# Kernel tuning notes

Measured on AMD Instinct MI355X. Metric: run time of the kernel, lower is better.

## Reference

```python
import jax, jax.numpy as jnp
import numpy as np

T, B, N = 512, 64, 1024
H = N // 2  # per-direction RNN hidden size


def _rnn_dir(x, Wih, Whh, bih, bhh):
    """Single-direction vanilla tanh RNN. x: [T,B,N] -> hs: [T,B,H]."""
    xw = jnp.einsum('tbn,hn->tbh', x, Wih) + bih  # precompute input proj
    h0 = jnp.zeros((x.shape[1], Whh.shape[0]), x.dtype)

    def step(hprev, xt):
        h = jnp.tanh(xt + hprev @ Whh.T + bhh)
        return h, h

    _, hs = jax.lax.scan(step, h0, xw)
    return hs


def setup_inputs() -> dict:
    key = jax.random.key(0)
    ks = jax.random.split(key, 8)
    sc_in = 1.0 / np.sqrt(N)
    sc_h = 1.0 / np.sqrt(H)
    return {
        's': jax.random.normal(ks[0], (B, N), jnp.float32),
        'x': jax.random.normal(ks[1], (T, B, N), jnp.float32),
        'Wih_f': jax.random.normal(ks[2], (H, N), jnp.float32) * sc_in,
        'Whh_f': jax.random.normal(ks[3], (H, H), jnp.float32) * sc_h,
        'bih_f': jnp.zeros((H,), jnp.float32),
        'bhh_f': jnp.zeros((H,), jnp.float32),
        'Wih_b': jax.random.normal(ks[4], (H, N), jnp.float32) * sc_in,
        'Whh_b': jax.random.normal(ks[5], (H, H), jnp.float32) * sc_h,
        'bih_b': jnp.zeros((H,), jnp.float32),
        'bhh_b': jnp.zeros((H,), jnp.float32),
        'W1': jax.random.normal(ks[6], (N, 2 * N), jnp.float32) * (1.0 / np.sqrt(2 * N)),
        'b1': jnp.zeros((N,), jnp.float32),
        'W2': jax.random.normal(ks[7], (1, N), jnp.float32) * sc_in,
        'b2': jnp.zeros((1,), jnp.float32),
    }


def reference(s, x, Wih_f, Whh_f, bih_f, bhh_f, Wih_b, Whh_b, bih_b, bhh_b, W1, b1, W2, b2):
    # Bidirectional RNN: forward scan + reversed scan, concat on feature axis.
    hf = _rnn_dir(x, Wih_f, Whh_f, bih_f, bhh_f)          # [T,B,H]
    hb = _rnn_dir(x[::-1], Wih_b, Whh_b, bih_b, bhh_b)[::-1]
    h = jnp.concatenate([hf, hb], axis=-1)                # [T,B,N]

    # Batched attention scoring MLP (replaces the per-timestep Python loop):
    # e_t = tanh(W2 @ tanh(W1 @ [s; h_t] + b1) + b2)
    sb = jnp.broadcast_to(s[None], h.shape)               # [T,B,N]
    z = jnp.concatenate([sb, h], axis=-1)                 # [T,B,2N]
    e = jnp.tanh(jnp.tanh(z @ W1.T + b1) @ W2.T + b2)     # [T,B,1]

    # softmax over time (original: softmax(dim=1) on [B,T]), then weighted sum.
    a = jax.nn.softmax(e[..., 0], axis=0)                 # [T,B]
    return jnp.einsum('tb,tbn->bn', a, h)                 # [B,N]
```

## Files before the change

kernel.cpp:

```cpp
#include <hip/hip_runtime.h>

#define Tn 512
#define Bn 64
#define Nn 1024
#define Hn 512

typedef __attribute__((ext_vector_type(8))) short short8;
typedef __attribute__((ext_vector_type(4))) float f32x4;
typedef __attribute__((ext_vector_type(4))) int int4v;

__device__ __forceinline__ unsigned short f2bf_hi(float x) {
  unsigned u = __builtin_bit_cast(unsigned, x);
  unsigned r = u + 0x7FFFu + ((u >> 16) & 1u);
  return (unsigned short)(r >> 16);
}
__device__ __forceinline__ float bf2f(unsigned short b) {
  unsigned u = ((unsigned)b) << 16;
  return __builtin_bit_cast(float, u);
}


__global__ __launch_bounds__(256) void k0_sproj(const float* __restrict__ s,
    const float* __restrict__ W1, const float* __restrict__ b1,
    float* __restrict__ SP) {
  const int b = blockIdx.x;
  const int tid = threadIdx.x;
  __shared__ float sl[Nn];
  for (int i = tid; i < Nn; i += 256) sl[i] = s[(size_t)b * Nn + i];
  __syncthreads();
#pragma unroll
  for (int qq = 0; qq < 4; ++qq) {
    const int j = qq * 256 + tid;
    const float* w = W1 + (size_t)j * (2 * Nn);
    float acc = 0.f;
    for (int i = 0; i < Nn; i += 4) {
      const float4 wv = *(const float4*)(w + i);
      acc += sl[i] * wv.x + sl[i + 1] * wv.y + sl[i + 2] * wv.z + sl[i + 3] * wv.w;
    }
    SP[(size_t)b * Nn + j] = acc + b1[j];
  }
}

#define LDA 40
__global__ __launch_bounds__(256) void k1_mfma(const float* __restrict__ X,
    const float* __restrict__ Wf, const float* __restrict__ Wb,
    const float* __restrict__ bif, const float* __restrict__ bib,
    float* __restrict__ XW) {
  __shared__ __align__(16) unsigned short Ahi[128 * LDA];
  __shared__ __align__(16) unsigned short Alo[128 * LDA];
  __shared__ __align__(16) unsigned short Bhi[128 * LDA];
  __shared__ __align__(16) unsigned short Blo[128 * LDA];
  const int tid = threadIdx.x;
  const int n0 = blockIdx.x * 128;
  const int m0 = blockIdx.y * 128;
  const int lane = tid & 63;
  const int w = tid >> 6;
  const int mw = (w >> 1) * 64, nw = (w & 1) * 64;
  const int l15 = lane & 15, l4 = lane >> 4;

  const float* bsrc;
  const float* bias_base;
  if (n0 < 512) { bsrc = Wf + (size_t)n0 * Nn; bias_base = bif + n0; }
  else          { bsrc = Wb + (size_t)(n0 - 512) * Nn; bias_base = bib + (n0 - 512); }

  const int srow = tid >> 1, scol = (tid & 1) * 16;
  const float* ag = X + (size_t)(m0 + srow) * Nn + scol;
  const float* bg = bsrc + (size_t)srow * Nn + scol;

  f32x4 acc[4][4];
#pragma unroll
  for (int i = 0; i < 4; ++i)
#pragma unroll
    for (int j = 0; j < 4; ++j) acc[i][j] = (f32x4){0.f, 0.f, 0.f, 0.f};

  for (int kt = 0; kt < 32; ++kt) {
    const int k0 = kt * 32;
    float4 av[4], bv[4];
#pragma unroll
    for (int c = 0; c < 4; ++c) {
      av[c] = *(const float4*)(ag + k0 + c * 4);
      bv[c] = *(const float4*)(bg + k0 + c * 4);
    }
    __syncthreads();
#pragma unroll
    for (int c = 0; c < 4; ++c) {
      const float a4[4] = {av[c].x, av[c].y, av[c].z, av[c].w};
      const float b4[4] = {bv[c].x, bv[c].y, bv[c].z, bv[c].w};
      ushort4 ah, al, bh, bl;
      unsigned short* ahp = (unsigned short*)&ah;
      unsigned short* alp = (unsigned short*)&al;
      unsigned short* bhp = (unsigned short*)&bh;
      unsigned short* blp = (unsigned short*)&bl;
#pragma unroll
      for (int e = 0; e < 4; ++e) {
        const unsigned short h = f2bf_hi(a4[e]);
        ahp[e] = h; alp[e] = f2bf_hi(a4[e] - bf2f(h));
        const unsigned short g = f2bf_hi(b4[e]);
        bhp[e] = g; blp[e] = f2bf_hi(b4[e] - bf2f(g));
      }
      const int off = srow * LDA + scol + c * 4;
      *(ushort4*)&Ahi[off] = ah; *(ushort4*)&Alo[off] = al;
      *(ushort4*)&Bhi[off] = bh; *(ushort4*)&Blo[off] = bl;
    }
    __syncthreads();
    short8 afh[4], afl[4];
#pragma unroll
    for (int mi = 0; mi < 4; ++mi) {
      const int off = (mw + mi * 16 + l15) * LDA + l4 * 8;
      afh[mi] = *(const short8*)&Ahi[off];
      afl[mi] = *(const short8*)&Alo[off];
    }
#pragma unroll
    for (int ni = 0; ni < 4; ++ni) {
      const int off = (nw + ni * 16 + l15) * LDA + l4 * 8;
      const short8 bfh = *(const short8*)&Bhi[off];
      const short8 bfl = *(const short8*)&Blo[off];
#pragma unroll
      for (int mi = 0; mi < 4; ++mi) {
        acc[mi][ni] = __builtin_amdgcn_mfma_f32_16x16x32_bf16(afh[mi], bfh, acc[mi][ni], 0, 0, 0);
        acc[mi][ni] = __builtin_amdgcn_mfma_f32_16x16x32_bf16(afh[mi], bfl, acc[mi][ni], 0, 0, 0);
        acc[mi][ni] = __builtin_amdgcn_mfma_f32_16x16x32_bf16(afl[mi], bfh, acc[mi][ni], 0, 0, 0);
      }
    }
  }
#pragma unroll
  for (int ni = 0; ni < 4; ++ni) {
    const int col = n0 + nw + ni * 16 + l15;
    const float bias = bias_base[nw + ni * 16 + l15];
#pragma unroll
    for (int mi = 0; mi < 4; ++mi) {
      const int row = m0 + mw + mi * 16 + l4 * 4;
#pragma unroll
      for (int reg = 0; reg < 4; ++reg)
        XW[(size_t)(row + reg) * Nn + col] = acc[mi][ni][reg] + bias;
    }
  }
}

#define K2F 16
#define WAITV8 do { asm volatile("s_waitcnt vmcnt(8)" ::: "memory"); __builtin_amdgcn_sched_barrier(0); } while (0)
#define WAITV0 do { asm volatile("s_waitcnt vmcnt(0)" ::: "memory"); __builtin_amdgcn_sched_barrier(0); } while (0)
#define K2_LD(dh, dl, kt) do { \
    const unsigned short* _ph = pbh + (size_t)(kt) * 2048; \
    const unsigned short* _pl = pbl + (size_t)(kt) * 2048; \
    asm volatile("global_load_dwordx4 %0, %1, off sc0 sc1" : "=v"(dh) : "v"(_ph)); \
    asm volatile("global_load_dwordx4 %0, %1, off sc0 sc1" : "=v"(dl) : "v"(_pl)); \
  } while (0)
#define K2_MM(xh, xl, kt) do { \
    const short8 _a = __builtin_bit_cast(short8, xh); \
    const short8 _c = __builtin_bit_cast(short8, xl); \
    a0 = __builtin_amdgcn_mfma_f32_16x16x32_bf16(_a, Bh[kt], a0, 0, 0, 0); \
    a1 = __builtin_amdgcn_mfma_f32_16x16x32_bf16(_a, Bl[kt], a1, 0, 0, 0); \
    a2 = __builtin_amdgcn_mfma_f32_16x16x32_bf16(_c, Bh[kt], a2, 0, 0, 0); \
  } while (0)

__global__ __launch_bounds__(512, 1) void k2_scan_mfma(
    const float* __restrict__ XW,
    const float* __restrict__ Whh_f, const float* __restrict__ Whh_b,
    const float* __restrict__ bhh_f, const float* __restrict__ bhh_b,
    unsigned short* __restrict__ HFhi, unsigned short* __restrict__ HFlo,
    int* __restrict__ FL) {
  const int wg = blockIdx.x;
  const int dir = wg >> 4;
  const int rg = wg & 15;
  const int tid = threadIdx.x;
  const int lane = tid & 63;
  const int w = tid >> 6;
  const int m = w & 3;
  const int cg = w >> 2;
  const int l15 = lane & 15, l4 = lane >> 4;
  __shared__ __align__(16) unsigned short PKhi[2048];
  __shared__ __align__(16) unsigned short PKlo[2048];

  const float* Whh = dir ? Whh_b : Whh_f;
  const float* bhh = dir ? bhh_b : bhh_f;
  const int ocol = rg * 32 + cg * 16 + l15;

  short8 Bh[16], Bl[16];
  {
    const float* wr = Whh + (size_t)ocol * Hn;
#pragma unroll
    for (int kt = 0; kt < 16; ++kt) {
      const float4 w0 = *(const float4*)(wr + kt * 32 + l4 * 8);
      const float4 w1 = *(const float4*)(wr + kt * 32 + l4 * 8 + 4);
      const float wf[8] = {w0.x, w0.y, w0.z, w0.w, w1.x, w1.y, w1.z, w1.w};
      union { unsigned short u[8]; short8 v; } hh, ll;
#pragma unroll
      for (int e = 0; e < 8; ++e) {
        const unsigned short h = f2bf_hi(wf[e]);
        hh.u[e] = h; ll.u[e] = f2bf_hi(wf[e] - bf2f(h));
      }
      Bh[kt] = hh.v; Bl[kt] = ll.v;
    }
  }
  const float bhh_c = bhh[ocol];
  const int g2p = cg * 2 + (l15 >> 3);
  const int ep = l15 & 7;

  for (int t = 0; t < Tn; ++t) {
    const int trow = dir ? (Tn - 1 - t) : t;
    float xw0, xw1, xw2, xw3;
    {
      const float* xp = XW + ((size_t)trow * Bn + m * 16 + l4 * 4) * Nn + dir * 512 + ocol;
      const float* x0 = xp;             const float* x1 = xp + Nn;
      const float* x2 = xp + 2 * Nn;    const float* x3 = xp + 3 * Nn;
      asm volatile("global_load_dword %0, %1, off" : "=v"(xw0) : "v"(x0));
      asm volatile("global_load_dword %0, %1, off" : "=v"(xw1) : "v"(x1));
      asm volatile("global_load_dword %0, %1, off" : "=v"(xw2) : "v"(x2));
      asm volatile("global_load_dword %0, %1, off" : "=v"(xw3) : "v"(x3));
    }

    f32x4 a0 = {0.f, 0.f, 0.f, 0.f}, a1 = a0, a2 = a0;
    if (t > 0) {
      {
        int* fp = FL + (size_t)(((dir << 9) | (t - 1))) * K2F;
        while (true) {
          const int v = __hip_atomic_load(fp + (lane & 15), __ATOMIC_RELAXED,
                                          __HIP_MEMORY_SCOPE_AGENT);
          if (__all(v != 0)) break;
          __builtin_amdgcn_s_sleep(1);
        }
      }
      asm volatile("" ::: "memory");
      const int hprow = dir ? (Tn - t) : (t - 1);
      const unsigned short* pbh =
          HFhi + (size_t)(hprow * 2 + dir) * 32768 + m * 512 + lane * 8;
      const unsigned short* pbl =
          HFlo + (size_t)(hprow * 2 + dir) * 32768 + m * 512 + lane * 8;
      int4v Ph[4], Pl[4], Qh[4], Ql[4];
      K2_LD(Ph[0], Pl[0], 0);  K2_LD(Ph[1], Pl[1], 1);
      K2_LD(Ph[2], Pl[2], 2);  K2_LD(Ph[3], Pl[3], 3);
      K2_LD(Qh[0], Ql[0], 4);  K2_LD(Qh[1], Ql[1], 5);
      K2_LD(Qh[2], Ql[2], 6);  K2_LD(Qh[3], Ql[3], 7);
      WAITV8;
      K2_MM(Ph[0], Pl[0], 0);  K2_MM(Ph[1], Pl[1], 1);
      K2_MM(Ph[2], Pl[2], 2);  K2_MM(Ph[3], Pl[3], 3);
      K2_LD(Ph[0], Pl[0], 8);  K2_LD(Ph[1], Pl[1], 9);
      K2_LD(Ph[2], Pl[2], 10); K2_LD(Ph[3], Pl[3], 11);
      WAITV8;
      K2_MM(Qh[0], Ql[0], 4);  K2_MM(Qh[1], Ql[1], 5);
      K2_MM(Qh[2], Ql[2], 6);  K2_MM(Qh[3], Ql[3], 7);
      K2_LD(Qh[0], Ql[0], 12); K2_LD(Qh[1], Ql[1], 13);
      K2_LD(Qh[2], Ql[2], 14); K2_LD(Qh[3], Ql[3], 15);
      WAITV8;
      K2_MM(Ph[0], Pl[0], 8);  K2_MM(Ph[1], Pl[1], 9);
      K2_MM(Ph[2], Pl[2], 10); K2_MM(Ph[3], Pl[3], 11);
      WAITV0;
      K2_MM(Qh[0], Ql[0], 12); K2_MM(Qh[1], Ql[1], 13);
      K2_MM(Qh[2], Ql[2], 14); K2_MM(Qh[3], Ql[3], 15);
    }
    WAITV0;

#pragma unroll
    for (int reg = 0; reg < 4; ++reg) {
      const float xwv = (reg == 0) ? xw0 : (reg == 1) ? xw1 : (reg == 2) ? xw2 : xw3;
      const float pre = a0[reg] + a1[reg] + a2[reg] + xwv + bhh_c;
      const float h = tanhf(pre);
      const unsigned short hi = f2bf_hi(h);
      const unsigned short lo = f2bf_hi(h - bf2f(hi));
      const int idx = m * 512 + g2p * 128 + (l4 * 4 + reg) * 8 + ep;
      PKhi[idx] = hi;
      PKlo[idx] = lo;
    }
    __syncthreads();
    {
      const int half = tid >> 8;
      const int i = tid & 255;
      unsigned short* dst = (half ? HFlo : HFhi) +
          (size_t)(trow * 2 + dir) * 32768 + (size_t)rg * 2048 + (size_t)i * 8;
      const unsigned short* src = (half ? PKlo : PKhi) + i * 8;
      const int4v v = *(const int4v*)src;
      asm volatile("global_store_dwordx4 %0, %1, off sc0 sc1" :: "v"(dst), "v"(v) : "memory");
    }
    asm volatile("s_waitcnt vmcnt(0)" ::: "memory");
    __syncthreads();
    if (tid == 0)
      __hip_atomic_store(FL + (size_t)(((dir << 9) | t)) * K2F + rg, 1,
                         __ATOMIC_RELAXED, __HIP_MEMORY_SCOPE_AGENT);
  }
}

__global__ __launch_bounds__(256) void k3_mfma(
    const unsigned short* __restrict__ Hhi, const unsigned short* __restrict__ Hlo,
    const float* __restrict__ W1, const float* __restrict__ SP,
    const float* __restrict__ W2, float* __restrict__ EP) {
  __shared__ __align__(16) unsigned short Ahi[128 * LDA];
  __shared__ __align__(16) unsigned short Alo[128 * LDA];
  __shared__ __align__(16) unsigned short Bhi[128 * LDA];
  __shared__ __align__(16) unsigned short Blo[128 * LDA];
  __shared__ __align__(16) float SPs[64 * 128];
  const int tid = threadIdx.x;
  const int n0 = blockIdx.x * 128;
  const int m0 = blockIdx.y * 128;
  const int lane = tid & 63;
  const int w = tid >> 6;
  const int mw = (w >> 1) * 64, nw = (w & 1) * 64;
  const int l15 = lane & 15, l4 = lane >> 4;

  {
    const int r64 = tid >> 2, c0 = (tid & 3) * 32;
    const float* sps = SP + (size_t)r64 * Nn + n0 + c0;
    float* spd = &SPs[r64 * 128 + c0];
#pragma unroll
    for (int c = 0; c < 8; ++c) *(float4*)(spd + c * 4) = *(const float4*)(sps + c * 4);
  }

  const int srow = tid >> 1, scol = (tid & 1) * 16;
  const int tb = m0 + srow;
  const int t3 = tb >> 6, b3 = tb & 63;
  const size_t abase = (size_t)t3 * 65536 + (size_t)(b3 >> 4) * 512 + (size_t)(b3 & 15) * 8
                     + (size_t)(scol >> 3) * 128;
  const float* bg = W1 + (size_t)(n0 + srow) * (2 * Nn) + Nn + scol;

  f32x4 acc[4][4];
#pragma unroll
  for (int i = 0; i < 4; ++i)
#pragma unroll
    for (int j = 0; j < 4; ++j) acc[i][j] = (f32x4){0.f, 0.f, 0.f, 0.f};

  for (int kt = 0; kt < 32; ++kt) {
    const int k0 = kt * 32;
    const size_t gidx = abase + (size_t)(kt >> 4) * 32768 + (size_t)(kt & 15) * 2048;
    const short8 avh0 = *(const short8*)(Hhi + gidx);
    const short8 avh1 = *(const short8*)(Hhi + gidx + 128);
    const short8 avl0 = *(const short8*)(Hlo + gidx);
    const short8 avl1 = *(const short8*)(Hlo + gidx + 128);
    float4 bv0 = *(const float4*)(bg + k0);
    float4 bv1 = *(const float4*)(bg + k0 + 4);
    float4 bv2 = *(const float4*)(bg + k0 + 8);
    float4 bv3 = *(const float4*)(bg + k0 + 12);
    __syncthreads();
    {
      const int off = srow * LDA + scol;
      *(short8*)&Ahi[off] = avh0; *(short8*)&Ahi[off + 8] = avh1;
      *(short8*)&Alo[off] = avl0; *(short8*)&Alo[off + 8] = avl1;
      const float b16[16] = {bv0.x, bv0.y, bv0.z, bv0.w, bv1.x, bv1.y, bv1.z, bv1.w,
                             bv2.x, bv2.y, bv2.z, bv2.w, bv3.x, bv3.y, bv3.z, bv3.w};
      union { unsigned short u[8]; short8 v; } bh0, bl0, bh1, bl1;
#pragma unroll
      for (int e = 0; e < 8; ++e) {
        unsigned short g = f2bf_hi(b16[e]);
        bh0.u[e] = g; bl0.u[e] = f2bf_hi(b16[e] - bf2f(g));
        g = f2bf_hi(b16[e + 8]);
        bh1.u[e] = g; bl1.u[e] = f2bf_hi(b16[e + 8] - bf2f(g));
      }
      *(short8*)&Bhi[off] = bh0.v; *(short8*)&Bhi[off + 8] = bh1.v;
      *(short8*)&Blo[off] = bl0.v; *(short8*)&Blo[off + 8] = bl1.v;
    }
    __syncthreads();
    short8 afh[4], afl[4];
#pragma unroll
    for (int mi = 0; mi < 4; ++mi) {
      const int off = (mw + mi * 16 + l15) * LDA + l4 * 8;
      afh[mi] = *(const short8*)&Ahi[off];
      afl[mi] = *(const short8*)&Alo[off];
    }
#pragma unroll
    for (int ni = 0; ni < 4; ++ni) {
      const int off = (nw + ni * 16 + l15) * LDA + l4 * 8;
      const short8 bfh = *(const short8*)&Bhi[off];
      const short8 bfl = *(const short8*)&Blo[off];
#pragma unroll
      for (int mi = 0; mi < 4; ++mi) {
        acc[mi][ni] = __builtin_amdgcn_mfma_f32_16x16x32_bf16(afh[mi], bfh, acc[mi][ni], 0, 0, 0);
        acc[mi][ni] = __builtin_amdgcn_mfma_f32_16x16x32_bf16(afh[mi], bfl, acc[mi][ni], 0, 0, 0);
        acc[mi][ni] = __builtin_amdgcn_mfma_f32_16x16x32_bf16(afl[mi], bfh, acc[mi][ni], 0, 0, 0);
      }
    }
  }
  float rs[4][4];
#pragma unroll
  for (int mi = 0; mi < 4; ++mi)
#pragma unroll
    for (int reg = 0; reg < 4; ++reg) rs[mi][reg] = 0.f;
#pragma unroll
  for (int ni = 0; ni < 4; ++ni) {
    const int col_l = nw + ni * 16 + l15;
    const float w2v = W2[n0 + col_l];
#pragma unroll
    for (int mi = 0; mi < 4; ++mi) {
      const int rl = mw + mi * 16 + l4 * 4;
#pragma unroll
      for (int reg = 0; reg < 4; ++reg) {
        const int b64 = (rl + reg) & 63;
        const float u = tanhf(acc[mi][ni][reg] + SPs[b64 * 128 + col_l]);
        rs[mi][reg] += u * w2v;
      }
    }
  }
#pragma unroll
  for (int mi = 0; mi < 4; ++mi)
#pragma unroll
    for (int reg = 0; reg < 4; ++reg) {
      float v = rs[mi][reg];
#pragma unroll
      for (int msk = 1; msk < 16; msk <<= 1) v += __shfl_xor(v, msk);
      if (l15 == 0)
        atomicAdd(EP + m0 + mw + mi * 16 + l4 * 4 + reg, v);
    }
}

__global__ __launch_bounds__(256) void k4_softmax(const float* __restrict__ EP,
    const float* __restrict__ b2, float* __restrict__ AA) {
  const int b = blockIdx.x;
  const int tid = threadIdx.x;
  __shared__ float rbuf[256];
  const float b2v = b2[0];
  const float v0 = tanhf(EP[(size_t)tid * Bn + b] + b2v);
  const float v1 = tanhf(EP[(size_t)(tid + 256) * Bn + b] + b2v);
  rbuf[tid] = fmaxf(v0, v1);
  __syncthreads();
  for (int off = 128; off > 0; off >>= 1) {
    if (tid < off) rbuf[tid] = fmaxf(rbuf[tid], rbuf[tid + off]);
    __syncthreads();
  }
  const float M = rbuf[0];
  __syncthreads();
  const float e0 = expf(v0 - M);
  const float e1 = expf(v1 - M);
  rbuf[tid] = e0 + e1;
  __syncthreads();
  for (int off = 128; off > 0; off >>= 1) {
    if (tid < off) rbuf[tid] = rbuf[tid] + rbuf[tid + off];
    __syncthreads();
  }
  const float S = rbuf[0];
  AA[(size_t)tid * Bn + b] = e0 / S;
  AA[(size_t)(tid + 256) * Bn + b] = e1 / S;
}

__global__ __launch_bounds__(256) void k5_out(const float* __restrict__ AA,
    const unsigned short* __restrict__ Hhi, const unsigned short* __restrict__ Hlo,
    float* __restrict__ out) {
  const int tid = threadIdx.x;
  const int bi = tid & 15;
  const int ns = tid >> 4;
  const int mb = blockIdx.x;
  const int b = mb * 16 + bi;
  const int n4 = blockIdx.y * 64 + ns * 4;
  const int p = n4;
  const size_t base = (size_t)(p >> 9) * 32768 + (size_t)((p & 511) >> 5) * 2048 +
                      (size_t)mb * 512 + (size_t)((p & 31) >> 3) * 128 +
                      (size_t)bi * 8 + (p & 7);
  float o0 = 0.f, o1 = 0.f, o2 = 0.f, o3 = 0.f;
  for (int t = 0; t < Tn; ++t) {
    const float a = AA[(size_t)t * Bn + b];
    const size_t idx = (size_t)t * 65536 + base;
    const ushort4 hi = *(const ushort4*)(Hhi + idx);
    const ushort4 lo = *(const ushort4*)(Hlo + idx);
    o0 += a * (bf2f(hi.x) + bf2f(lo.x));
    o1 += a * (bf2f(hi.y) + bf2f(lo.y));
    o2 += a * (bf2f(hi.z) + bf2f(lo.z));
    o3 += a * (bf2f(hi.w) + bf2f(lo.w));
  }
  float* op = out + (size_t)b * Nn + n4;
  op[0] = o0; op[1] = o1; op[2] = o2; op[3] = o3;
}

extern "C" void kernel_launch(void* const* d_in, const int* in_sizes, int n_in,
                              void* d_out, int out_size, void* d_ws, size_t ws_size,
                              hipStream_t stream) {
  const float* s     = (const float*)d_in[0];
  const float* x     = (const float*)d_in[1];
  const float* Wih_f = (const float*)d_in[2];
  const float* Whh_f = (const float*)d_in[3];
  const float* bih_f = (const float*)d_in[4];
  const float* bhh_f = (const float*)d_in[5];
  const float* Wih_b = (const float*)d_in[6];
  const float* Whh_b = (const float*)d_in[7];
  const float* bih_b = (const float*)d_in[8];
  const float* bhh_b = (const float*)d_in[9];
  const float* W1    = (const float*)d_in[10];
  const float* b1    = (const float*)d_in[11];
  const float* W2    = (const float*)d_in[12];
  const float* b2    = (const float*)d_in[13];
  float* out = (float*)d_out;

  float* XW = (float*)d_ws;
  unsigned short* Hhi = (unsigned short*)(XW + 33554432ULL);
  unsigned short* Hlo = Hhi + 33554432ULL;
  float* SP = (float*)(Hlo + 33554432ULL);
  float* EP = SP + 65536ULL;
  float* AA = EP + 32768ULL;
  int* FL   = (int*)(AA + 32768ULL);
  const size_t need = 33554432ULL * 4 + 33554432ULL * 2 * 2 +
                      (65536ULL + 32768 + 32768) * 4 + 16384ULL * 4;
  if (ws_size < need) return;

  hipMemsetAsync(EP, 0, 32768 * sizeof(float), stream);
  hipMemsetAsync(FL, 0, 16384 * sizeof(int), stream);

  k0_sproj<<<dim3(64), 256, 0, stream>>>(s, W1, b1, SP);
  k1_mfma<<<dim3(8, 256), 256, 0, stream>>>(x, Wih_f, Wih_b, bih_f, bih_b, XW);
  k2_scan_mfma<<<dim3(32), 512, 0, stream>>>(XW, Whh_f, Whh_b, bhh_f, bhh_b, Hhi, Hlo, FL);
  k3_mfma<<<dim3(8, 256), 256, 0, stream>>>(Hhi, Hlo, W1, SP, W2, EP);
  k4_softmax<<<dim3(64), 256, 0, stream>>>(EP, b2, AA);
  k5_out<<<dim3(4, 16), 256, 0, stream>>>(AA, Hhi, Hlo, out);
}
```

Baseline: 2.976 ms.

## Pin recurrent scan workgroups to a single XCD and relax cache bypass

The scan kernel now launches 256 workgroups. Each reads its XCD id from a hardware register and counts arrivals per XCD, and the first XCD to collect 32 blocks claims the 32 scan roles while every other block exits. With all cooperating workgroups on one XCD sharing an L2, the h-state stores drop the sc0 sc1 bits and the loads drop sc1. Only one wave per block polls the step flags now, followed by a block barrier. This aims to cut the per-timestep cross-XCD coherence latency, at the cost of extra launched blocks, an election spin, and a dependence on the hardware dispatching enough blocks to each XCD.

New measurement: 3.416 ms. 14.8% more time.

```diff
diff --git a/kernel.cpp b/kernel.cpp
--- a/kernel.cpp
+++ b/kernel.cpp
@@ -143,8 +143,8 @@
 #define K2_LD(dh, dl, kt) do { \
     const unsigned short* _ph = pbh + (size_t)(kt) * 2048; \
     const unsigned short* _pl = pbl + (size_t)(kt) * 2048; \
-    asm volatile("global_load_dwordx4 %0, %1, off sc0 sc1" : "=v"(dh) : "v"(_ph)); \
-    asm volatile("global_load_dwordx4 %0, %1, off sc0 sc1" : "=v"(dl) : "v"(_pl)); \
+    asm volatile("global_load_dwordx4 %0, %1, off sc0" : "=v"(dh) : "v"(_ph)); \
+    asm volatile("global_load_dwordx4 %0, %1, off sc0" : "=v"(dl) : "v"(_pl)); \
   } while (0)
 #define K2_MM(xh, xl, kt) do { \
     const short8 _a = __builtin_bit_cast(short8, xh); \
@@ -159,11 +159,30 @@
     const float* __restrict__ Whh_f, const float* __restrict__ Whh_b,
     const float* __restrict__ bhh_f, const float* __restrict__ bhh_b,
     unsigned short* __restrict__ HFhi, unsigned short* __restrict__ HFlo,
-    int* __restrict__ FL) {
-  const int wg = blockIdx.x;
-  const int dir = wg >> 4;
-  const int rg = wg & 15;
+    int* __restrict__ FL, int* __restrict__ CL) {
   const int tid = threadIdx.x;
+  __shared__ int role_s;
+  if (tid == 0) {
+    const int xcd = __builtin_amdgcn_s_getreg(6164) & 7;
+    const int r = __hip_atomic_fetch_add(&CL[xcd], 1, __ATOMIC_RELAXED,
+                                         __HIP_MEMORY_SCOPE_AGENT);
+    if (r == 31) {
+      int expected = 0;
+      __hip_atomic_compare_exchange_strong(&CL[8], &expected, xcd + 1,
+          __ATOMIC_RELAXED, __ATOMIC_RELAXED, __HIP_MEMORY_SCOPE_AGENT);
+    }
+    int h;
+    while ((h = __hip_atomic_load(&CL[8], __ATOMIC_RELAXED,
+                                  __HIP_MEMORY_SCOPE_AGENT)) == 0)
+      __builtin_amdgcn_s_sleep(8);
+    role_s = (h - 1 == xcd && r < 32) ? r : -1;
+  }
+  __syncthreads();
+  const int role = role_s;
+  if (role < 0) return;
+
+  const int dir = role >> 4;
+  const int rg = role & 15;
   const int lane = tid & 63;
   const int w = tid >> 6;
   const int m = w & 3;
@@ -212,15 +231,16 @@
 
     f32x4 a0 = {0.f, 0.f, 0.f, 0.f}, a1 = a0, a2 = a0;
     if (t > 0) {
-      {
+      if (tid < 64) {
         int* fp = FL + (size_t)(((dir << 9) | (t - 1))) * K2F;
         while (true) {
-          const int v = __hip_atomic_load(fp + (lane & 15), __ATOMIC_RELAXED,
+          const int v = __hip_atomic_load(fp + (tid & 15), __ATOMIC_RELAXED,
                                           __HIP_MEMORY_SCOPE_AGENT);
           if (__all(v != 0)) break;
           __builtin_amdgcn_s_sleep(1);
         }
       }
+      __syncthreads();
       asm volatile("" ::: "memory");
       const int hprow = dir ? (Tn - t) : (t - 1);
       const unsigned short* pbh =
@@ -270,7 +290,7 @@
           (size_t)(trow * 2 + dir) * 32768 + (size_t)rg * 2048 + (size_t)i * 8;
       const unsigned short* src = (half ? PKlo : PKhi) + i * 8;
       const int4v v = *(const int4v*)src;
-      asm volatile("global_store_dwordx4 %0, %1, off sc0 sc1" :: "v"(dst), "v"(v) : "memory");
+      asm volatile("global_store_dwordx4 %0, %1, off" :: "v"(dst), "v"(v) : "memory");
     }
     asm volatile("s_waitcnt vmcnt(0)" ::: "memory");
     __syncthreads();
@@ -483,16 +503,17 @@
   float* EP = SP + 65536ULL;
   float* AA = EP + 32768ULL;
   int* FL   = (int*)(AA + 32768ULL);
+  int* CL   = FL + 16384ULL;
   const size_t need = 33554432ULL * 4 + 33554432ULL * 2 * 2 +
-                      (65536ULL + 32768 + 32768) * 4 + 16384ULL * 4;
+                      (65536ULL + 32768 + 32768) * 4 + (16384ULL + 16) * 4;
   if (ws_size < need) return;
 
   hipMemsetAsync(EP, 0, 32768 * sizeof(float), stream);
-  hipMemsetAsync(FL, 0, 16384 * sizeof(int), stream);
+  hipMemsetAsync(FL, 0, (16384 + 16) * sizeof(int), stream);
 
   k0_sproj<<<dim3(64), 256, 0, stream>>>(s, W1, b1, SP);
   k1_mfma<<<dim3(8, 256), 256, 0, stream>>>(x, Wih_f, Wih_b, bih_f, bih_b, XW);
-  k2_scan_mfma<<<dim3(32), 512, 0, stream>>>(XW, Whh_f, Whh_b, bhh_f, bhh_b, Hhi, Hlo, FL);
+  k2_scan_mfma<<<dim3(256), 512, 0, stream>>>(XW, Whh_f, Whh_b, bhh_f, bhh_b, Hhi, Hlo, FL, CL);
   k3_mfma<<<dim3(8, 256), 256, 0, stream>>>(Hhi, Hlo, W1, SP, W2, EP);
   k4_softmax<<<dim3(64), 256, 0, stream>>>(EP, b2, AA);
   k5_out<<<dim3(4, 16), 256, 0, stream>>>(AA, Hhi, Hlo, out);
```
